# Performance work log

Measured on AMD Instinct MI355X. Metric: run time of the kernel, lower is better.

## Reference

```python
import jax, jax.numpy as jnp
import numpy as np

B, LQ, LK, NF = 8, 8192, 1024, 64


def setup_inputs() -> dict:
    key = jax.random.key(0)
    k1, k2, k3, k4, k5 = jax.random.split(key, 5)
    x = jax.random.normal(k1, (B, LQ, NF), dtype=jnp.float32)
    kv = jax.random.normal(k2, (B, LK, NF), dtype=jnp.float32)
    # 1x1 submanifold convolutions == per-point linear maps (no bias)
    scale = 1.0 / np.sqrt(NF)
    Wq = jax.random.normal(k3, (NF, NF), dtype=jnp.float32) * scale
    Wk = jax.random.normal(k4, (NF, NF), dtype=jnp.float32) * scale
    Wv = jax.random.normal(k5, (NF, NF), dtype=jnp.float32) * scale
    return {"x": x, "kv": kv, "Wq": Wq, "Wk": Wk, "Wv": Wv}


def reference(x, kv, Wq, Wk, Wv):
    # q/k/v projections (1x1 convs on sparse features = dense matmuls)
    q = jnp.einsum("bqd,de->bqe", x, Wq)    # [B, LQ, NF]
    k = jnp.einsum("bkd,de->bke", kv, Wk)   # [B, LK, NF]
    v = jnp.einsum("bkd,de->bke", kv, Wv)   # [B, LK, NF]
    # per-batch (block-diagonal / ragged) attention: e = q k^T, softmax over keys, @ v
    scores = jnp.einsum("bqe,bke->bqk", q, k)        # [B, LQ, LK] (no scaling, as in source)
    attn = jax.nn.softmax(scores, axis=-1)
    out = jnp.einsum("bqk,bke->bqe", attn, v)        # [B, LQ, NF]
    return out
```

## Files before the change

kernel.cpp:

```cpp
#include <hip/hip_runtime.h>
#include <hip/hip_fp16.h>

constexpr int B_  = 8;
constexpr int LQ  = 8192;
constexpr int LK  = 1024;
constexpr int NF  = 64;
constexpr int PAD = 8;
constexpr int LDW = NF + PAD;

typedef _Float16 f16x8 __attribute__((ext_vector_type(8)));
typedef float    f32x4 __attribute__((ext_vector_type(4)));

#define MFMA16(a, b, c) __builtin_amdgcn_mfma_f32_16x16x32_f16((a), (b), (c), 0, 0, 0)

__device__ __forceinline__ f16x8 cvt8(const float* p) {
  float4 a = ((const float4*)p)[0];
  float4 b = ((const float4*)p)[1];
  f16x8 r;
  r[0] = (_Float16)a.x; r[1] = (_Float16)a.y; r[2] = (_Float16)a.z; r[3] = (_Float16)a.w;
  r[4] = (_Float16)b.x; r[5] = (_Float16)b.y; r[6] = (_Float16)b.z; r[7] = (_Float16)b.w;
  return r;
}

__device__ __forceinline__ f16x8 ldf(const _Float16* p) { return *(const f16x8*)p; }

__device__ __forceinline__ void st_pk4(_Float16* dst, float a, float b, float c, float d) {
  auto lo = __builtin_amdgcn_cvt_pkrtz(a, b);
  auto hi = __builtin_amdgcn_cvt_pkrtz(c, d);
  auto v  = __builtin_shufflevector(lo, hi, 0, 1, 2, 3);
  *(decltype(v)*)dst = v;
}

__device__ __forceinline__ f16x8 pack8(f32x4 u, f32x4 v) {
  auto a = __builtin_amdgcn_cvt_pkrtz(u[0], u[1]);
  auto b = __builtin_amdgcn_cvt_pkrtz(u[2], u[3]);
  auto cc = __builtin_amdgcn_cvt_pkrtz(v[0], v[1]);
  auto d = __builtin_amdgcn_cvt_pkrtz(v[2], v[3]);
  f16x8 r;
  r[0] = a[0]; r[1] = a[1]; r[2] = b[0];  r[3] = b[1];
  r[4] = cc[0]; r[5] = cc[1]; r[6] = d[0]; r[7] = d[1];
  return r;
}

__global__ __launch_bounds__(256) void kv_proj_kernel(
    const float* __restrict__ kv, const float* __restrict__ Wk,
    const float* __restrict__ Wv, _Float16* __restrict__ Kb,
    _Float16* __restrict__ Vt) {
  __shared__ __align__(16) _Float16 wkT[NF][LDW];
  __shared__ __align__(16) _Float16 wvT[NF][LDW];
  __shared__ __align__(16) _Float16 ktile[64][LDW];
  __shared__ __align__(16) _Float16 vtileT[64][LDW];

  const int t    = threadIdx.x;
  const int wave = t >> 6, lane = t & 63, g = lane >> 4, c = lane & 15;
  const int b    = blockIdx.x >> 4;
  const int key_base = (blockIdx.x & 15) * 64;

#pragma unroll
  for (int i = 0; i < 16; ++i) {
    int idx = t + 256 * i;
    int e = idx >> 6, d = idx & 63;
    wkT[d][e] = (_Float16)Wk[idx];
    wvT[d][e] = (_Float16)Wv[idx];
  }

  const float* src = kv + ((size_t)b * LK + key_base + wave * 16 + c) * NF;
  f16x8 a0 = cvt8(src + g * 8);
  f16x8 a1 = cvt8(src + 32 + g * 8);
  __syncthreads();

#pragma unroll
  for (int mb = 0; mb < 4; ++mb) {
    f32x4 kacc = {0.f, 0.f, 0.f, 0.f};
    const _Float16* wk0 = &wkT[mb * 16 + c][g * 8];
    kacc = MFMA16(ldf(wk0),      a0, kacc);
    kacc = MFMA16(ldf(wk0 + 32), a1, kacc);
    st_pk4(&ktile[wave * 16 + c][(8 * (mb >> 1) + 2 * g + (mb & 1)) * 4],
           kacc[0], kacc[1], kacc[2], kacc[3]);

    f32x4 vacc = {0.f, 0.f, 0.f, 0.f};
    const _Float16* wv0 = &wvT[mb * 16 + c][g * 8];
    vacc = MFMA16(a0, ldf(wv0),      vacc);
    vacc = MFMA16(a1, ldf(wv0 + 32), vacc);
    st_pk4(&vtileT[mb * 16 + c][(8 * (wave >> 1) + 2 * g + (wave & 1)) * 4],
           vacc[0], vacc[1], vacc[2], vacc[3]);
  }
  __syncthreads();

  const int srow = t >> 2, scol = (t & 3) * 16;
  {
    float4* kd = (float4*)(Kb + ((size_t)b * LK + key_base + srow) * NF + scol);
    kd[0] = *(float4*)&ktile[srow][scol];
    kd[1] = *(float4*)&ktile[srow][scol + 8];
    float4* vd = (float4*)(Vt + ((size_t)b * NF + srow) * LK + key_base + scol);
    vd[0] = *(float4*)&vtileT[srow][scol];
    vd[1] = *(float4*)&vtileT[srow][scol + 8];
  }
}

__global__ __launch_bounds__(128, 4) void attn_kernel(
    const float* __restrict__ x, const float* __restrict__ Wq,
    const _Float16* __restrict__ Kb, const _Float16* __restrict__ Vt,
    float* __restrict__ out) {
  __shared__ __align__(16) _Float16 ks[64][LDW];
  __shared__ __align__(16) _Float16 vs[64][LDW];

  const int t    = threadIdx.x;
  const int wave = t >> 6, lane = t & 63, g = lane >> 4, c = lane & 15;
  const int b    = blockIdx.x >> 7;
  const int q_base = (blockIdx.x & 127) * 64;
  constexpr float LOG2E = 1.44269504088896f;

#pragma unroll
  for (int i = 0; i < 32; ++i) {
    int idx = t + 128 * i;
    ks[idx & 63][idx >> 6] = (_Float16)(Wq[idx] * LOG2E);
  }

  const _Float16* Kg = Kb + (size_t)b * LK * NF;
  const _Float16* Vg = Vt + (size_t)b * NF * LK;
  const int srow = t >> 1, shalf = t & 1;

  f16x8 kpre[4];
  {
    const f16x8* kp = (const f16x8*)(Kg + srow * NF + shalf * 32);
    kpre[0] = kp[0]; kpre[1] = kp[1]; kpre[2] = kp[2]; kpre[3] = kp[3];
  }
  __syncthreads();

  f16x8 qb[2][2];
#pragma unroll
  for (int s = 0; s < 2; ++s) {
    const float* xrow = x + ((size_t)b * LQ + q_base + wave * 32 + s * 16 + c) * NF;
    f16x8 xa0 = cvt8(xrow + g * 8);
    f16x8 xa1 = cvt8(xrow + 32 + g * 8);
    f32x4 qa[4];
#pragma unroll
    for (int mb = 0; mb < 4; ++mb) {
      qa[mb] = {0.f, 0.f, 0.f, 0.f};
      const _Float16* wq0 = &ks[mb * 16 + c][g * 8];
      qa[mb] = MFMA16(ldf(wq0),      xa0, qa[mb]);
      qa[mb] = MFMA16(ldf(wq0 + 32), xa1, qa[mb]);
    }
    qb[s][0] = pack8(qa[0], qa[1]);
    qb[s][1] = pack8(qa[2], qa[3]);
  }
  __syncthreads();

  float m_s[2] = {-1e30f, -1e30f}, l_s[2] = {0.f, 0.f};
  f32x4 oacc[2][4];
#pragma unroll
  for (int s = 0; s < 2; ++s)
#pragma unroll
    for (int nb = 0; nb < 4; ++nb) oacc[s][nb] = {0.f, 0.f, 0.f, 0.f};

  for (int tile = 0; tile < 16; ++tile) {
    *(f16x8*)&ks[srow][shalf * 32]      = kpre[0];
    *(f16x8*)&ks[srow][shalf * 32 + 8]  = kpre[1];
    *(f16x8*)&ks[srow][shalf * 32 + 16] = kpre[2];
    *(f16x8*)&ks[srow][shalf * 32 + 24] = kpre[3];
    {
      const f16x8* vp = (const f16x8*)(Vg + (size_t)srow * LK + tile * 64 + shalf * 32);
      f16x8 v0 = vp[0], v1 = vp[1], v2 = vp[2], v3 = vp[3];
      *(f16x8*)&vs[srow][shalf * 32]      = v0;
      *(f16x8*)&vs[srow][shalf * 32 + 8]  = v1;
      *(f16x8*)&vs[srow][shalf * 32 + 16] = v2;
      *(f16x8*)&vs[srow][shalf * 32 + 24] = v3;
    }
    __syncthreads();
    if (tile < 15) {
      const f16x8* kp = (const f16x8*)(Kg + (size_t)(tile + 1) * 64 * NF + srow * NF + shalf * 32);
      kpre[0] = kp[0]; kpre[1] = kp[1]; kpre[2] = kp[2]; kpre[3] = kp[3];
    }

    f32x4 st[2][4];
#pragma unroll
    for (int kb = 0; kb < 4; ++kb) {
      const _Float16* kf = &ks[kb * 16 + c][g * 8];
      f16x8 k0 = ldf(kf), k1 = ldf(kf + 32);
      st[0][kb] = {0.f, 0.f, 0.f, 0.f};
      st[1][kb] = {0.f, 0.f, 0.f, 0.f};
      st[0][kb] = MFMA16(k0, qb[0][0], st[0][kb]);
      st[0][kb] = MFMA16(k1, qb[0][1], st[0][kb]);
      st[1][kb] = MFMA16(k0, qb[1][0], st[1][kb]);
      st[1][kb] = MFMA16(k1, qb[1][1], st[1][kb]);
    }

    f16x8 pa[2][2];
#pragma unroll
    for (int s = 0; s < 2; ++s) {
      float tmax = st[s][0][0];
#pragma unroll
      for (int kb = 0; kb < 4; ++kb)
#pragma unroll
        for (int r = 0; r < 4; ++r) tmax = fmaxf(tmax, st[s][kb][r]);
      tmax = fmaxf(tmax, __shfl_xor(tmax, 16));
      tmax = fmaxf(tmax, __shfl_xor(tmax, 32));

      if (__ballot(tmax > m_s[s]) != 0) {
        float mnew  = fmaxf(m_s[s], tmax);
        float alpha = __builtin_amdgcn_exp2f(m_s[s] - mnew);
        m_s[s] = mnew;
        l_s[s] *= alpha;
        float aq[4];
#pragma unroll
        for (int r = 0; r < 4; ++r) aq[r] = __shfl(alpha, 4 * g + r);
#pragma unroll
        for (int nb = 0; nb < 4; ++nb)
#pragma unroll
          for (int r = 0; r < 4; ++r) oacc[s][nb][r] *= aq[r];
      }

      float rsum = 0.f;
#pragma unroll
      for (int kb = 0; kb < 4; ++kb)
#pragma unroll
        for (int r = 0; r < 4; ++r) {
          float p = __builtin_amdgcn_exp2f(st[s][kb][r] - m_s[s]);
          st[s][kb][r] = p;
          rsum += p;
        }
      rsum += __shfl_xor(rsum, 16);
      rsum += __shfl_xor(rsum, 32);
      l_s[s] += rsum;

      pa[s][0] = pack8(st[s][0], st[s][1]);
      pa[s][1] = pack8(st[s][2], st[s][3]);
    }

#pragma unroll
    for (int nb = 0; nb < 4; ++nb) {
      const _Float16* vf = &vs[nb * 16 + c][g * 8];
      f16x8 v0 = ldf(vf), v1 = ldf(vf + 32);
      oacc[0][nb] = MFMA16(pa[0][0], v0, oacc[0][nb]);
      oacc[0][nb] = MFMA16(pa[0][1], v1, oacc[0][nb]);
      oacc[1][nb] = MFMA16(pa[1][0], v0, oacc[1][nb]);
      oacc[1][nb] = MFMA16(pa[1][1], v1, oacc[1][nb]);
    }
    __syncthreads();
  }

#pragma unroll
  for (int s = 0; s < 2; ++s) {
    float linv = 1.0f / l_s[s];
    float lq[4];
#pragma unroll
    for (int r = 0; r < 4; ++r) lq[r] = __shfl(linv, 4 * g + r);
#pragma unroll
    for (int nb = 0; nb < 4; ++nb)
#pragma unroll
      for (int r = 0; r < 4; ++r)
        out[((size_t)b * LQ + q_base + wave * 32 + s * 16 + 4 * g + r) * NF + nb * 16 + c] =
            oacc[s][nb][r] * lq[r];
  }
}

extern "C" void kernel_launch(void* const* d_in, const int* in_sizes, int n_in,
                              void* d_out, int out_size, void* d_ws, size_t ws_size,
                              hipStream_t stream) {
  const float* x  = (const float*)d_in[0];
  const float* kv = (const float*)d_in[1];
  const float* Wq = (const float*)d_in[2];
  const float* Wk = (const float*)d_in[3];
  const float* Wv = (const float*)d_in[4];
  float* out = (float*)d_out;

  _Float16* Kb = (_Float16*)d_ws;
  _Float16* Vt = Kb + (size_t)B_ * LK * NF;

  kv_proj_kernel<<<B_ * (LK / 64), 256, 0, stream>>>(kv, Wk, Wv, Kb, Vt);
  attn_kernel<<<B_ * (LQ / 64), 128, 0, stream>>>(x, Wq, Kb, Vt, out);
}
```

Baseline: 110.6 us.

## Load K/V MFMA fragments directly from global into registers, drop LDS staging

The attention kernel no longer stages K and V tiles through shared memory. Each wave loads its MFMA operand fragments for K and V straight from global memory into registers and prefetches the next tile's fragments after use, which removes the per-tile barriers. The block grows to 256 threads covering 128 queries, with 4 waves each streaming K/V independently. This cuts LDS traffic and synchronisation, but every wave now issues redundant global/L2 loads for the same K/V data, and register pressure rises.

Result: slower. 136.2 us (+23.1%).

```diff
diff --git a/kernel.cpp b/kernel.cpp
--- a/kernel.cpp
+++ b/kernel.cpp
@@ -32,12 +32,12 @@
 }
 
 __device__ __forceinline__ f16x8 pack8(f32x4 u, f32x4 v) {
-  auto a = __builtin_amdgcn_cvt_pkrtz(u[0], u[1]);
-  auto b = __builtin_amdgcn_cvt_pkrtz(u[2], u[3]);
+  auto a  = __builtin_amdgcn_cvt_pkrtz(u[0], u[1]);
+  auto b  = __builtin_amdgcn_cvt_pkrtz(u[2], u[3]);
   auto cc = __builtin_amdgcn_cvt_pkrtz(v[0], v[1]);
-  auto d = __builtin_amdgcn_cvt_pkrtz(v[2], v[3]);
+  auto d  = __builtin_amdgcn_cvt_pkrtz(v[2], v[3]);
   f16x8 r;
-  r[0] = a[0]; r[1] = a[1]; r[2] = b[0];  r[3] = b[1];
+  r[0] = a[0];  r[1] = a[1];  r[2] = b[0]; r[3] = b[1];
   r[4] = cc[0]; r[5] = cc[1]; r[6] = d[0]; r[7] = d[1];
   return r;
 }
@@ -98,33 +98,34 @@
   }
 }
 
-__global__ __launch_bounds__(128, 4) void attn_kernel(
+__global__ __launch_bounds__(256) void attn_kernel(
     const float* __restrict__ x, const float* __restrict__ Wq,
     const _Float16* __restrict__ Kb, const _Float16* __restrict__ Vt,
     float* __restrict__ out) {
-  __shared__ __align__(16) _Float16 ks[64][LDW];
-  __shared__ __align__(16) _Float16 vs[64][LDW];
+  __shared__ __align__(16) _Float16 wq[NF][LDW];
 
   const int t    = threadIdx.x;
   const int wave = t >> 6, lane = t & 63, g = lane >> 4, c = lane & 15;
-  const int b    = blockIdx.x >> 7;
-  const int q_base = (blockIdx.x & 127) * 64;
+  const int b    = blockIdx.x >> 6;
+  const int q_base = (blockIdx.x & 63) * 128;
   constexpr float LOG2E = 1.44269504088896f;
 
 #pragma unroll
-  for (int i = 0; i < 32; ++i) {
-    int idx = t + 128 * i;
-    ks[idx & 63][idx >> 6] = (_Float16)(Wq[idx] * LOG2E);
+  for (int i = 0; i < 16; ++i) {
+    int idx = t + 256 * i;
+    wq[idx & 63][idx >> 6] = (_Float16)(Wq[idx] * LOG2E);
   }
 
   const _Float16* Kg = Kb + (size_t)b * LK * NF;
   const _Float16* Vg = Vt + (size_t)b * NF * LK;
-  const int srow = t >> 1, shalf = t & 1;
-
-  f16x8 kpre[4];
-  {
-    const f16x8* kp = (const f16x8*)(Kg + srow * NF + shalf * 32);
-    kpre[0] = kp[0]; kpre[1] = kp[1]; kpre[2] = kp[2]; kpre[3] = kp[3];
+
+  f16x8 kf[8], vf[8];
+#pragma unroll
+  for (int kb = 0; kb < 4; ++kb) {
+    const _Float16* p = Kg + (kb * 16 + c) * NF + g * 8;
+    kf[2 * kb] = ldf(p); kf[2 * kb + 1] = ldf(p + 32);
+    const _Float16* q = Vg + (size_t)(kb * 16 + c) * LK + g * 8;
+    vf[2 * kb] = ldf(q); vf[2 * kb + 1] = ldf(q + 32);
   }
   __syncthreads();
 
@@ -138,14 +139,13 @@
 #pragma unroll
     for (int mb = 0; mb < 4; ++mb) {
       qa[mb] = {0.f, 0.f, 0.f, 0.f};
-      const _Float16* wq0 = &ks[mb * 16 + c][g * 8];
+      const _Float16* wq0 = &wq[mb * 16 + c][g * 8];
       qa[mb] = MFMA16(ldf(wq0),      xa0, qa[mb]);
       qa[mb] = MFMA16(ldf(wq0 + 32), xa1, qa[mb]);
     }
     qb[s][0] = pack8(qa[0], qa[1]);
     qb[s][1] = pack8(qa[2], qa[3]);
   }
-  __syncthreads();
 
   float m_s[2] = {-1e30f, -1e30f}, l_s[2] = {0.f, 0.f};
   f32x4 oacc[2][4];
@@ -154,36 +154,25 @@
 #pragma unroll
     for (int nb = 0; nb < 4; ++nb) oacc[s][nb] = {0.f, 0.f, 0.f, 0.f};
 
+#pragma unroll 2
   for (int tile = 0; tile < 16; ++tile) {
-    *(f16x8*)&ks[srow][shalf * 32]      = kpre[0];
-    *(f16x8*)&ks[srow][shalf * 32 + 8]  = kpre[1];
-    *(f16x8*)&ks[srow][shalf * 32 + 16] = kpre[2];
-    *(f16x8*)&ks[srow][shalf * 32 + 24] = kpre[3];
-    {
-      const f16x8* vp = (const f16x8*)(Vg + (size_t)srow * LK + tile * 64 + shalf * 32);
-      f16x8 v0 = vp[0], v1 = vp[1], v2 = vp[2], v3 = vp[3];
-      *(f16x8*)&vs[srow][shalf * 32]      = v0;
-      *(f16x8*)&vs[srow][shalf * 32 + 8]  = v1;
-      *(f16x8*)&vs[srow][shalf * 32 + 16] = v2;
-      *(f16x8*)&vs[srow][shalf * 32 + 24] = v3;
-    }
-    __syncthreads();
-    if (tile < 15) {
-      const f16x8* kp = (const f16x8*)(Kg + (size_t)(tile + 1) * 64 * NF + srow * NF + shalf * 32);
-      kpre[0] = kp[0]; kpre[1] = kp[1]; kpre[2] = kp[2]; kpre[3] = kp[3];
-    }
-
     f32x4 st[2][4];
 #pragma unroll
     for (int kb = 0; kb < 4; ++kb) {
-      const _Float16* kf = &ks[kb * 16 + c][g * 8];
-      f16x8 k0 = ldf(kf), k1 = ldf(kf + 32);
       st[0][kb] = {0.f, 0.f, 0.f, 0.f};
       st[1][kb] = {0.f, 0.f, 0.f, 0.f};
-      st[0][kb] = MFMA16(k0, qb[0][0], st[0][kb]);
-      st[0][kb] = MFMA16(k1, qb[0][1], st[0][kb]);
-      st[1][kb] = MFMA16(k0, qb[1][0], st[1][kb]);
-      st[1][kb] = MFMA16(k1, qb[1][1], st[1][kb]);
+      st[0][kb] = MFMA16(kf[2 * kb], qb[0][0], st[0][kb]);
+      st[0][kb] = MFMA16(kf[2 * kb + 1], qb[0][1], st[0][kb]);
+      st[1][kb] = MFMA16(kf[2 * kb], qb[1][0], st[1][kb]);
+      st[1][kb] = MFMA16(kf[2 * kb + 1], qb[1][1], st[1][kb]);
+    }
+    if (tile < 15) {
+      const _Float16* kn = Kg + (size_t)(tile + 1) * 64 * NF;
+#pragma unroll
+      for (int kb = 0; kb < 4; ++kb) {
+        const _Float16* p = kn + (kb * 16 + c) * NF + g * 8;
+        kf[2 * kb] = ldf(p); kf[2 * kb + 1] = ldf(p + 32);
+      }
     }
 
     f16x8 pa[2][2];
@@ -230,14 +219,18 @@
 
 #pragma unroll
     for (int nb = 0; nb < 4; ++nb) {
-      const _Float16* vf = &vs[nb * 16 + c][g * 8];
-      f16x8 v0 = ldf(vf), v1 = ldf(vf + 32);
-      oacc[0][nb] = MFMA16(pa[0][0], v0, oacc[0][nb]);
-      oacc[0][nb] = MFMA16(pa[0][1], v1, oacc[0][nb]);
-      oacc[1][nb] = MFMA16(pa[1][0], v0, oacc[1][nb]);
-      oacc[1][nb] = MFMA16(pa[1][1], v1, oacc[1][nb]);
-    }
-    __syncthreads();
+      oacc[0][nb] = MFMA16(pa[0][0], vf[2 * nb],     oacc[0][nb]);
+      oacc[0][nb] = MFMA16(pa[0][1], vf[2 * nb + 1], oacc[0][nb]);
+      oacc[1][nb] = MFMA16(pa[1][0], vf[2 * nb],     oacc[1][nb]);
+      oacc[1][nb] = MFMA16(pa[1][1], vf[2 * nb + 1], oacc[1][nb]);
+    }
+    if (tile < 15) {
+#pragma unroll
+      for (int nb = 0; nb < 4; ++nb) {
+        const _Float16* p = Vg + (size_t)(nb * 16 + c) * LK + (tile + 1) * 64 + g * 8;
+        vf[2 * nb] = ldf(p); vf[2 * nb + 1] = ldf(p + 32);
+      }
+    }
   }
 
 #pragma unroll
@@ -269,5 +262,5 @@
   _Float16* Vt = Kb + (size_t)B_ * LK * NF;
 
   kv_proj_kernel<<<B_ * (LK / 64), 256, 0, stream>>>(kv, Wk, Wv, Kb, Vt);
-  attn_kernel<<<B_ * (LQ / 64), 128, 0, stream>>>(x, Wq, Kb, Vt, out);
-}
+  attn_kernel<<<B_ * (LQ / 128), 256, 0, stream>>>(x, Wq, Kb, Vt, out);
+}
```
